# Kernel tuning notes

Hardware: AMD Instinct MI355X
Metric: run time of the kernel (lower is better)

Reference implementation:

```python
import jax, jax.numpy as jnp
import numpy as np

N = 4096
NUM_FEATURES = 1870
HIDDEN = 256
EMBED = 16
ALPHA = 0.2
NEG_BIG = -9e15
EPS = 1e-12


def setup_inputs() -> dict:
    key = jax.random.key(0)
    ks = jax.random.split(key, 9)
    x = jax.random.normal(ks[0], (N, NUM_FEATURES), dtype=jnp.float32)
    # sparse-ish binary adjacency mask (avg degree ~ 41) with self loops
    adj = (jax.random.uniform(ks[1], (N, N)) < 0.01).astype(jnp.float32)
    adj = jnp.maximum(adj, jnp.eye(N, dtype=jnp.float32))
    M = jax.random.uniform(ks[2], (N, N), dtype=jnp.float32)
    s1 = 1.0 / np.sqrt(NUM_FEATURES)
    s2 = 1.0 / np.sqrt(HIDDEN)
    W1 = jax.random.normal(ks[3], (NUM_FEATURES, HIDDEN), dtype=jnp.float32) * s1
    a_self1 = jax.random.normal(ks[4], (HIDDEN, 1), dtype=jnp.float32) * s2
    a_neighs1 = jax.random.normal(ks[5], (HIDDEN, 1), dtype=jnp.float32) * s2
    W2 = jax.random.normal(ks[6], (HIDDEN, EMBED), dtype=jnp.float32) * s2
    a_self2 = jax.random.normal(ks[7], (EMBED, 1), dtype=jnp.float32) / np.sqrt(EMBED)
    a_neighs2 = jax.random.normal(ks[8], (EMBED, 1), dtype=jnp.float32) / np.sqrt(EMBED)
    return {"x": x, "adj": adj, "M": M, "W1": W1, "a_self1": a_self1,
            "a_neighs1": a_neighs1, "W2": W2, "a_self2": a_self2, "a_neighs2": a_neighs2}


def gat_layer(x, adj, M, W, a_self, a_neighs, alpha):
    h = x @ W                                  # [N, out]
    f_self = h @ a_self                        # [N, 1]
    f_neigh = h @ a_neighs                     # [N, 1]
    e = jax.nn.leaky_relu((f_self + f_neigh.T) * M, negative_slope=alpha)  # [N, N]
    e = jnp.where(adj > 0, e, NEG_BIG)
    att = jax.nn.softmax(e, axis=1)            # row-stochastic over neighbors
    return jax.nn.elu(att @ h)                 # [N, out]


def reference(x, adj, M, W1, a_self1, a_neighs1, W2, a_self2, a_neighs2):
    h = gat_layer(x, adj, M, W1, a_self1, a_neighs1, ALPHA)
    h = gat_layer(h, adj, M, W2, a_self2, a_neighs2, ALPHA)
    # F.normalize(h, p=2, dim=1): divide by max(norm, eps)
    norm = jnp.maximum(jnp.linalg.norm(h, axis=1, keepdims=True), EPS)
    z = h / norm                               # [N, EMBED]
    A_pred = jax.nn.sigmoid(z @ z.T)           # [N, N]
    return (A_pred, z)
```

## Files before the change

kernel.cpp:

```cpp
#include <hip/hip_runtime.h>
#include <math.h>

#define NN 4096
#define NFEAT 1870
#define KB 1920
#define KSPLIT 4
#define KCHUNK 480
#define NSTEP 15
#define HID 256
#define EMB 16
#define MAXDEG 128

typedef __attribute__((ext_vector_type(8))) _Float16 f16x8;
typedef __attribute__((ext_vector_type(4))) float f32x4;

__device__ __forceinline__ ushort f2h(float f) {
    _Float16 h = (_Float16)f;
    return __builtin_bit_cast(ushort, h);
}

struct af32 { float2 v[4]; };

__device__ __forceinline__ af32 load_a_raw(const float* __restrict__ rp, int k0) {
    af32 r;
    if (k0 + 8 <= NFEAT) {
#pragma unroll
        for (int j = 0; j < 4; ++j) r.v[j] = *(const float2*)&rp[k0 + j * 2];
    } else {
#pragma unroll
        for (int j = 0; j < 4; ++j) {
            float a = (k0 + j * 2     < NFEAT) ? rp[k0 + j * 2]     : 0.f;
            float b = (k0 + j * 2 + 1 < NFEAT) ? rp[k0 + j * 2 + 1] : 0.f;
            r.v[j] = make_float2(a, b);
        }
    }
    return r;
}
__device__ __forceinline__ f16x8 cvt_a(af32 r) {
    f16x8 o;
#pragma unroll
    for (int j = 0; j < 4; ++j) {
        o[j * 2]     = (_Float16)r.v[j].x;
        o[j * 2 + 1] = (_Float16)r.v[j].y;
    }
    return o;
}

__global__ __launch_bounds__(256) void prep_kernel(
    const float* __restrict__ W1, ushort* __restrict__ Wh,
    const float* __restrict__ adj, const float* __restrict__ Mmat,
    int* __restrict__ nnz, int* __restrict__ gidx, float* __restrict__ Mg)
{
    const int b = blockIdx.x;
    const int tid = threadIdx.x;
    if (b < NN) {
        const int row = b;
        const int lane = tid & 63, wv = tid >> 6;
        const float* arow = adj + (size_t)row * NN + tid * 16;
        float4 v[4];
#pragma unroll
        for (int i = 0; i < 4; ++i) v[i] = *(const float4*)&arow[i * 4];
        unsigned mask = 0;
#pragma unroll
        for (int i = 0; i < 4; ++i) {
            if (v[i].x > 0.f) mask |= 1u << (i * 4 + 0);
            if (v[i].y > 0.f) mask |= 1u << (i * 4 + 1);
            if (v[i].z > 0.f) mask |= 1u << (i * 4 + 2);
            if (v[i].w > 0.f) mask |= 1u << (i * 4 + 3);
        }
        const int cnt = __popc(mask);
        int incl = cnt;
#pragma unroll
        for (int off = 1; off < 64; off <<= 1) {
            int y = __shfl_up(incl, off, 64);
            if (lane >= off) incl += y;
        }
        __shared__ int wsums[4];
        if (lane == 63) wsums[wv] = incl;
        __syncthreads();
        int base = incl - cnt;
#pragma unroll
        for (int i = 0; i < 4; ++i)
            if (i < wv) base += wsums[i];
        if (tid == 0) {
            int total = wsums[0] + wsums[1] + wsums[2] + wsums[3];
            nnz[row] = min(total, MAXDEG);
        }
        unsigned mm = mask;
        int off = base;
        while (mm) {
            int bit = __ffs(mm) - 1;
            mm &= mm - 1;
            if (off < MAXDEG) {
                int j = tid * 16 + bit;
                gidx[(size_t)row * MAXDEG + off] = j;
                Mg[(size_t)row * MAXDEG + off] = Mmat[(size_t)row * NN + j];
            }
            ++off;
        }
    } else {
        __shared__ float t[64][65];
        const int bb = b - NN;
        const int k0 = (bb % 30) * 64, n0 = (bb / 30) * 64;
        const int kk = tid >> 2, c4 = (tid & 3) * 16;
#pragma unroll
        for (int j = 0; j < 4; ++j) {
            int k = k0 + kk;
            float4 v = make_float4(0.f, 0.f, 0.f, 0.f);
            if (k < NFEAT) v = *(const float4*)&W1[(size_t)k * HID + n0 + c4 + j * 4];
            t[kk][c4 + j * 4 + 0] = v.x; t[kk][c4 + j * 4 + 1] = v.y;
            t[kk][c4 + j * 4 + 2] = v.z; t[kk][c4 + j * 4 + 3] = v.w;
        }
        __syncthreads();
        const int on = tid >> 2, ok4 = (tid & 3) * 16;
#pragma unroll
        for (int j = 0; j < 4; ++j) {
            ushort hh[4];
#pragma unroll
            for (int i = 0; i < 4; ++i)
                hh[i] = f2h(t[ok4 + j * 4 + i][on]);
            size_t o = (size_t)(n0 + on) * KB + k0 + ok4 + j * 4;
            *(ushort4*)&Wh[o] = *(ushort4*)hh;
        }
    }
}

__global__ __launch_bounds__(256, 4) void gemm_xw1(
    const float* __restrict__ Xg,
    const ushort* __restrict__ Bg,
    float* __restrict__ Cpart)
{
    const int tid = threadIdx.x;
    const int lane = tid & 63;
    const int cgrp = tid >> 6;
    const int mgrp = blockIdx.x >> 2;
    const int z    = blockIdx.x & 3;
    const int row0 = mgrp * 16;
    const int col0 = cgrp * 64;
    const int kbeg = z * KCHUNK;
    const int fr = lane & 15, fs = lane >> 4;

    const float* Arow = Xg + (size_t)(row0 + fr) * NFEAT;
    const ushort* Bbase = Bg + (size_t)(col0 + fr) * KB + kbeg + fs * 8;

    af32 araw = load_a_raw(Arow, kbeg + fs * 8);
    f16x8 bc[4];
#pragma unroll
    for (int n = 0; n < 4; ++n)
        bc[n] = *(const f16x8*)&Bbase[(size_t)n * 16 * KB];

    f32x4 acc[4] = {};
#pragma unroll
    for (int sk = 0; sk < NSTEP; ++sk) {
        f16x8 ac = cvt_a(araw);
        af32 anxt;
        f16x8 bn[4];
        if (sk + 1 < NSTEP) {
            anxt = load_a_raw(Arow, kbeg + (sk + 1) * 32 + fs * 8);
#pragma unroll
            for (int n = 0; n < 4; ++n)
                bn[n] = *(const f16x8*)&Bbase[(size_t)n * 16 * KB + (sk + 1) * 32];
        }
#pragma unroll
        for (int n = 0; n < 4; ++n)
            acc[n] = __builtin_amdgcn_mfma_f32_16x16x32_f16(ac, bc[n], acc[n], 0, 0, 0);
        if (sk + 1 < NSTEP) {
            araw = anxt;
#pragma unroll
            for (int n = 0; n < 4; ++n) bc[n] = bn[n];
        }
    }
    float* Cp = Cpart + (size_t)z * NN * HID;
#pragma unroll
    for (int n = 0; n < 4; ++n)
#pragma unroll
        for (int r = 0; r < 4; ++r) {
            int row = row0 + fs * 4 + r;
            int col = col0 + n * 16 + fr;
            Cp[(size_t)row * HID + col] = acc[n][r];
        }
}

__global__ __launch_bounds__(256) void reduce_h1f_kernel(
    const float* __restrict__ part, float* __restrict__ h1,
    const float* __restrict__ a_s, const float* __restrict__ a_n,
    float* __restrict__ fs, float* __restrict__ fn)
{
    const int tid = threadIdx.x, wv = tid >> 6, lane = tid & 63;
    const int row = blockIdx.x * 4 + wv;
    const int d0 = lane * 4;
    const size_t o = (size_t)row * HID + d0;
    float4 s = *(const float4*)&part[o];
#pragma unroll
    for (int ch = 1; ch < KSPLIT; ++ch) {
        float4 p = *(const float4*)&part[(size_t)ch * NN * HID + o];
        s.x += p.x; s.y += p.y; s.z += p.z; s.w += p.w;
    }
    *(float4*)&h1[o] = s;
    float4 as4 = *(const float4*)&a_s[d0];
    float4 an4 = *(const float4*)&a_n[d0];
    float ps = s.x * as4.x + s.y * as4.y + s.z * as4.z + s.w * as4.w;
    float pn = s.x * an4.x + s.y * an4.y + s.z * an4.z + s.w * an4.w;
#pragma unroll
    for (int off = 32; off > 0; off >>= 1) {
        ps += __shfl_down(ps, off, 64);
        pn += __shfl_down(pn, off, 64);
    }
    if (lane == 0) { fs[row] = ps; fn[row] = pn; }
}

__global__ __launch_bounds__(256) void spmm1_kernel(
    const int* __restrict__ nnz, const int* __restrict__ gidx,
    const float* __restrict__ Mg,
    const float* __restrict__ fs, const float* __restrict__ fn,
    const float* __restrict__ h1, float* __restrict__ g1)
{
    __shared__ float p_s[MAXDEG];
    __shared__ int j_s[MAXDEG];
    __shared__ float wred[4], wsum[4];
    const int row = blockIdx.x;
    const int tid = threadIdx.x;
    const int lane = tid & 63, wv = tid >> 6;
    const int cnt = nnz[row];
    const float fsi = fs[row];

    float lmax = -3.0e38f;
    for (int s = tid; s < cnt; s += 256) {
        int j = gidx[(size_t)row * MAXDEG + s];
        j_s[s] = j;
        float e = (fsi + fn[j]) * Mg[(size_t)row * MAXDEG + s];
        e = (e > 0.f) ? e : 0.2f * e;
        p_s[s] = e;
        lmax = fmaxf(lmax, e);
    }
#pragma unroll
    for (int off = 32; off > 0; off >>= 1)
        lmax = fmaxf(lmax, __shfl_down(lmax, off, 64));
    if (lane == 0) wred[wv] = lmax;
    __syncthreads();
    const float m = fmaxf(fmaxf(wred[0], wred[1]), fmaxf(wred[2], wred[3]));

    float lsum = 0.f;
    for (int s = tid; s < cnt; s += 256) {
        float p = __expf(p_s[s] - m);
        p_s[s] = p;
        lsum += p;
    }
#pragma unroll
    for (int off = 32; off > 0; off >>= 1)
        lsum += __shfl_down(lsum, off, 64);
    if (lane == 0) wsum[wv] = lsum;
    __syncthreads();
    const float inv = 1.f / (wsum[0] + wsum[1] + wsum[2] + wsum[3]);

    float acc = 0.f;
#pragma unroll 4
    for (int s = 0; s < cnt; ++s)
        acc += p_s[s] * h1[(size_t)j_s[s] * HID + tid];
    float v = acc * inv;
    v = (v > 0.f) ? v : (__expf(v) - 1.f);
    g1[(size_t)row * HID + tid] = v;
}

__global__ __launch_bounds__(256) void gemm_h2_kernel(
    const float* __restrict__ g1, const float* __restrict__ W2,
    const float* __restrict__ a_s2, const float* __restrict__ a_n2,
    float* __restrict__ h2, float* __restrict__ fs2, float* __restrict__ fn2)
{
    __shared__ float Ws[256][16];
    __shared__ float Gs[16][257];
    const int tid = threadIdx.x;
    const int row0 = blockIdx.x * 16;
#pragma unroll
    for (int i = 0; i < 16; ++i) {
        int idx = tid + i * 256;
        Ws[idx >> 4][idx & 15] = W2[idx];
    }
#pragma unroll
    for (int i = 0; i < 16; ++i) {
        int idx = tid + i * 256;
        Gs[idx >> 8][idx & 255] = g1[(size_t)(row0 + (idx >> 8)) * HID + (idx & 255)];
    }
    __syncthreads();
    const int r = tid >> 4, c = tid & 15;
    float acc = 0.f;
#pragma unroll 8
    for (int k = 0; k < 256; ++k)
        acc += Gs[r][k] * Ws[k][c];
    h2[(size_t)(row0 + r) * EMB + c] = acc;

    float ps = acc * a_s2[c];
    float pn = acc * a_n2[c];
#pragma unroll
    for (int off = 1; off < 16; off <<= 1) {
        ps += __shfl_xor(ps, off, 64);
        pn += __shfl_xor(pn, off, 64);
    }
    if (c == 0) { fs2[row0 + r] = ps; fn2[row0 + r] = pn; }
}

__global__ __launch_bounds__(256) void spmm2_kernel(
    const int* __restrict__ nnz, const int* __restrict__ gidx,
    const float* __restrict__ Mg,
    const float* __restrict__ fs, const float* __restrict__ fn,
    const float* __restrict__ h2, float* __restrict__ z)
{
    __shared__ float p_s[4][MAXDEG];
    __shared__ int j_s[4][MAXDEG];
    const int tid = threadIdx.x;
    const int wv = tid >> 6, lane = tid & 63;
    const int row = blockIdx.x * 4 + wv;
    const int cnt = nnz[row];
    const float fsi = fs[row];

    float lmax = -3.0e38f;
    for (int s = lane; s < cnt; s += 64) {
        int j = gidx[(size_t)row * MAXDEG + s];
        j_s[wv][s] = j;
        float e = (fsi + fn[j]) * Mg[(size_t)row * MAXDEG + s];
        e = (e > 0.f) ? e : 0.2f * e;
        p_s[wv][s] = e;
        lmax = fmaxf(lmax, e);
    }
#pragma unroll
    for (int off = 1; off < 64; off <<= 1)
        lmax = fmaxf(lmax, __shfl_xor(lmax, off, 64));

    float lsum = 0.f;
    for (int s = lane; s < cnt; s += 64) {
        float p = __expf(p_s[wv][s] - lmax);
        p_s[wv][s] = p;
        lsum += p;
    }
#pragma unroll
    for (int off = 1; off < 64; off <<= 1)
        lsum += __shfl_xor(lsum, off, 64);
    const float inv = 1.f / lsum;

    const int s0 = lane >> 4, d = lane & 15;
    float acc = 0.f;
    for (int s = s0; s < cnt; s += 4)
        acc += p_s[wv][s] * h2[(size_t)j_s[wv][s] * EMB + d];
    acc += __shfl_xor(acc, 16, 64);
    acc += __shfl_xor(acc, 32, 64);

    float v = acc * inv;
    v = (v > 0.f) ? v : (__expf(v) - 1.f);
    float ss = v * v;
#pragma unroll
    for (int off = 1; off < 16; off <<= 1)
        ss += __shfl_xor(ss, off, 64);
    float zn = v / fmaxf(sqrtf(ss), 1e-12f);
    if (lane < 16) z[(size_t)row * EMB + lane] = zn;
}

__global__ __launch_bounds__(256) void apred_kernel(
    const float* __restrict__ z, float* __restrict__ out)
{
    __shared__ float zr[64][20];
    __shared__ float zc[64][20];
    const int tid = threadIdx.x;
    const int r0 = blockIdx.y * 64, c0 = blockIdx.x * 64;
#pragma unroll
    for (int i = 0; i < 4; ++i) {
        int idx = tid + i * 256;
        int rr = idx >> 4, d = idx & 15;
        zr[rr][d] = z[(size_t)(r0 + rr) * EMB + d];
        zc[rr][d] = z[(size_t)(c0 + rr) * EMB + d];
    }
    __syncthreads();
    const int tx = tid & 15, ty = tid >> 4;
    float rb[4][16], cb[4][16];
#pragma unroll
    for (int i = 0; i < 4; ++i)
#pragma unroll
        for (int d = 0; d < 16; ++d) {
            rb[i][d] = zr[ty * 4 + i][d];
            cb[i][d] = zc[tx * 4 + i][d];
        }
#pragma unroll
    for (int i = 0; i < 4; ++i) {
        float4 o;
        float v[4];
#pragma unroll
        for (int j = 0; j < 4; ++j) {
            float s = 0.f;
#pragma unroll
            for (int d = 0; d < 16; ++d) s += rb[i][d] * cb[j][d];
            v[j] = 1.f / (1.f + __expf(-s));
        }
        o.x = v[0]; o.y = v[1]; o.z = v[2]; o.w = v[3];
        *reinterpret_cast<float4*>(
            &out[(size_t)(r0 + ty * 4 + i) * NN + c0 + tx * 4]) = o;
    }
}

extern "C" void kernel_launch(void* const* d_in, const int* in_sizes, int n_in,
                              void* d_out, int out_size, void* d_ws, size_t ws_size,
                              hipStream_t stream)
{
    const float* x    = (const float*)d_in[0];
    const float* adj  = (const float*)d_in[1];
    const float* Mm   = (const float*)d_in[2];
    const float* W1   = (const float*)d_in[3];
    const float* a_s1 = (const float*)d_in[4];
    const float* a_n1 = (const float*)d_in[5];
    const float* W2   = (const float*)d_in[6];
    const float* a_s2 = (const float*)d_in[7];
    const float* a_n2 = (const float*)d_in[8];

    float* out = (float*)d_out;
    float* z   = out + (size_t)NN * NN;
    float* part = out;

    char* w = (char*)d_ws;
    float* h1    = (float*)w;  w += (size_t)NN * HID * 4;
    float* g1    = (float*)w;  w += (size_t)NN * HID * 4;
    ushort* W1Th = (ushort*)w; w += (size_t)HID * KB * 2;
    float* h2    = (float*)w;  w += (size_t)NN * EMB * 4;
    int*   nnzp  = (int*)w;    w += NN * 4;
    int*   gidx  = (int*)w;    w += (size_t)NN * MAXDEG * 4;
    float* Mg    = (float*)w;  w += (size_t)NN * MAXDEG * 4;
    float* fs1   = (float*)w;  w += NN * 4;
    float* fn1   = (float*)w;  w += NN * 4;
    float* fs2   = (float*)w;  w += NN * 4;
    float* fn2   = (float*)w;  w += NN * 4;

    prep_kernel<<<NN + 120, 256, 0, stream>>>(W1, W1Th, adj, Mm, nnzp, gidx, Mg);

    gemm_xw1<<<(NN / 16) * KSPLIT, 256, 0, stream>>>(x, W1Th, part);
    reduce_h1f_kernel<<<NN / 4, 256, 0, stream>>>(part, h1, a_s1, a_n1, fs1, fn1);
    spmm1_kernel<<<NN, 256, 0, stream>>>(nnzp, gidx, Mg, fs1, fn1, h1, g1);

    gemm_h2_kernel<<<256, 256, 0, stream>>>(g1, W2, a_s2, a_n2, h2, fs2, fn2);
    spmm2_kernel<<<NN / 4, 256, 0, stream>>>(nnzp, gidx, Mg, fs2, fn2, h2, z);

    apred_kernel<<<dim3(64, 64), 256, 0, stream>>>(z, out);
}
```

Measured before the change: 109.9 us.

## Pre-convert x to fp16 and use LDS-tiled 128x128 split-K MFMA GEMM

```diff
diff --git a/kernel.cpp b/kernel.cpp
--- a/kernel.cpp
+++ b/kernel.cpp
@@ -3,10 +3,10 @@
 
 #define NN 4096
 #define NFEAT 1870
-#define KB 1920
-#define KSPLIT 4
-#define KCHUNK 480
-#define NSTEP 15
+#define KB2 2048
+#define KSPLIT 8
+#define KCHUNK 256
+#define BK 32
 #define HID 256
 #define EMB 16
 #define MAXDEG 128
@@ -19,34 +19,14 @@
     return __builtin_bit_cast(ushort, h);
 }
 
-struct af32 { float2 v[4]; };
-
-__device__ __forceinline__ af32 load_a_raw(const float* __restrict__ rp, int k0) {
-    af32 r;
-    if (k0 + 8 <= NFEAT) {
-#pragma unroll
-        for (int j = 0; j < 4; ++j) r.v[j] = *(const float2*)&rp[k0 + j * 2];
-    } else {
-#pragma unroll
-        for (int j = 0; j < 4; ++j) {
-            float a = (k0 + j * 2     < NFEAT) ? rp[k0 + j * 2]     : 0.f;
-            float b = (k0 + j * 2 + 1 < NFEAT) ? rp[k0 + j * 2 + 1] : 0.f;
-            r.v[j] = make_float2(a, b);
-        }
-    }
-    return r;
-}
-__device__ __forceinline__ f16x8 cvt_a(af32 r) {
-    f16x8 o;
-#pragma unroll
-    for (int j = 0; j < 4; ++j) {
-        o[j * 2]     = (_Float16)r.v[j].x;
-        o[j * 2 + 1] = (_Float16)r.v[j].y;
-    }
-    return o;
+__device__ __forceinline__ void gload_lds16(const void* g, void* l) {
+    __builtin_amdgcn_global_load_lds(
+        (const __attribute__((address_space(1))) unsigned int*)g,
+        (__attribute__((address_space(3))) unsigned int*)l, 16, 0, 0);
 }
 
 __global__ __launch_bounds__(256) void prep_kernel(
+    const float* __restrict__ x, ushort* __restrict__ xf,
     const float* __restrict__ W1, ushort* __restrict__ Wh,
     const float* __restrict__ adj, const float* __restrict__ Mmat,
     int* __restrict__ nnz, int* __restrict__ gidx, float* __restrict__ Mg)
@@ -98,10 +78,29 @@
             }
             ++off;
         }
+    } else if (b < 2 * NN) {
+        const int row = b - NN;
+        const int c0 = tid * 8;
+        float v[8];
+        if (c0 + 8 <= NFEAT) {
+#pragma unroll
+            for (int j = 0; j < 4; ++j) {
+                float2 t = *(const float2*)&x[(size_t)row * NFEAT + c0 + j * 2];
+                v[j * 2] = t.x; v[j * 2 + 1] = t.y;
+            }
+        } else {
+#pragma unroll
+            for (int j = 0; j < 8; ++j)
+                v[j] = (c0 + j < NFEAT) ? x[(size_t)row * NFEAT + c0 + j] : 0.f;
+        }
+        ushort u[8];
+#pragma unroll
+        for (int j = 0; j < 8; ++j) u[j] = f2h(v[j]);
+        *(int4*)&xf[(size_t)row * KB2 + c0] = *(int4*)u;
     } else {
         __shared__ float t[64][65];
-        const int bb = b - NN;
-        const int k0 = (bb % 30) * 64, n0 = (bb / 30) * 64;
+        const int bb = b - 2 * NN;
+        const int k0 = (bb & 31) * 64, n0 = (bb >> 5) * 64;
         const int kk = tid >> 2, c4 = (tid & 3) * 16;
 #pragma unroll
         for (int j = 0; j < 4; ++j) {
@@ -119,66 +118,71 @@
 #pragma unroll
             for (int i = 0; i < 4; ++i)
                 hh[i] = f2h(t[ok4 + j * 4 + i][on]);
-            size_t o = (size_t)(n0 + on) * KB + k0 + ok4 + j * 4;
+            size_t o = (size_t)(n0 + on) * KB2 + k0 + ok4 + j * 4;
             *(ushort4*)&Wh[o] = *(ushort4*)hh;
         }
     }
 }
 
-__global__ __launch_bounds__(256, 4) void gemm_xw1(
-    const float* __restrict__ Xg,
+__global__ __launch_bounds__(256, 2) void gemm_xw1(
+    const ushort* __restrict__ Ag,
     const ushort* __restrict__ Bg,
     float* __restrict__ Cpart)
 {
+    __shared__ ushort Ah[128 * BK];
+    __shared__ ushort Bh[128 * BK];
     const int tid = threadIdx.x;
     const int lane = tid & 63;
-    const int cgrp = tid >> 6;
-    const int mgrp = blockIdx.x >> 2;
-    const int z    = blockIdx.x & 3;
-    const int row0 = mgrp * 16;
-    const int col0 = cgrp * 64;
-    const int kbeg = z * KCHUNK;
+    const int w = tid >> 6;
+    const int wr = w >> 1, wc = w & 1;
+    const int row0 = blockIdx.x * 128;
+    const int col0 = blockIdx.y * 128;
+    const int kbeg = blockIdx.z * KCHUNK;
     const int fr = lane & 15, fs = lane >> 4;
 
-    const float* Arow = Xg + (size_t)(row0 + fr) * NFEAT;
-    const ushort* Bbase = Bg + (size_t)(col0 + fr) * KB + kbeg + fs * 8;
-
-    af32 araw = load_a_raw(Arow, kbeg + fs * 8);
-    f16x8 bc[4];
-#pragma unroll
-    for (int n = 0; n < 4; ++n)
-        bc[n] = *(const f16x8*)&Bbase[(size_t)n * 16 * KB];
-
-    f32x4 acc[4] = {};
-#pragma unroll
-    for (int sk = 0; sk < NSTEP; ++sk) {
-        f16x8 ac = cvt_a(araw);
-        af32 anxt;
-        f16x8 bn[4];
-        if (sk + 1 < NSTEP) {
-            anxt = load_a_raw(Arow, kbeg + (sk + 1) * 32 + fs * 8);
+    f32x4 acc[4][4] = {};
+
+    for (int ks = 0; ks < KCHUNK / BK; ++ks) {
+        const int k0 = kbeg + ks * BK;
+        __syncthreads();
+#pragma unroll
+        for (int i = 0; i < 2; ++i) {
+            int idx = i * 256 + tid;
+            int r = idx >> 2, t = idx & 3;
+            int kslot = (t ^ (r & 3)) * 8;
+            gload_lds16(&Ag[(size_t)(row0 + r) * KB2 + k0 + kslot], &Ah[idx * 8]);
+            gload_lds16(&Bg[(size_t)(col0 + r) * KB2 + k0 + kslot], &Bh[idx * 8]);
+        }
+        __syncthreads();
+        f16x8 af[4], bf[4];
+#pragma unroll
+        for (int m = 0; m < 4; ++m) {
+            int r = wr * 64 + m * 16 + fr;
+            af[m] = *(const f16x8*)&Ah[r * BK + ((fs ^ (r & 3)) * 8)];
+        }
+#pragma unroll
+        for (int n = 0; n < 4; ++n) {
+            int r = wc * 64 + n * 16 + fr;
+            bf[n] = *(const f16x8*)&Bh[r * BK + ((fs ^ (r & 3)) * 8)];
+        }
+#pragma unroll
+        for (int m = 0; m < 4; ++m)
 #pragma unroll
             for (int n = 0; n < 4; ++n)
-                bn[n] = *(const f16x8*)&Bbase[(size_t)n * 16 * KB + (sk + 1) * 32];
-        }
+                acc[m][n] = __builtin_amdgcn_mfma_f32_16x16x32_f16(
+                    af[m], bf[n], acc[m][n], 0, 0, 0);
+    }
+    float* Cp = Cpart + (size_t)blockIdx.z * NN * HID;
+#pragma unroll
+    for (int m = 0; m < 4; ++m)
 #pragma unroll
         for (int n = 0; n < 4; ++n)
-            acc[n] = __builtin_amdgcn_mfma_f32_16x16x32_f16(ac, bc[n], acc[n], 0, 0, 0);
-        if (sk + 1 < NSTEP) {
-            araw = anxt;
-#pragma unroll
-            for (int n = 0; n < 4; ++n) bc[n] = bn[n];
-        }
-    }
-    float* Cp = Cpart + (size_t)z * NN * HID;
-#pragma unroll
-    for (int n = 0; n < 4; ++n)
-#pragma unroll
-        for (int r = 0; r < 4; ++r) {
-            int row = row0 + fs * 4 + r;
-            int col = col0 + n * 16 + fr;
-            Cp[(size_t)row * HID + col] = acc[n][r];
-        }
+#pragma unroll
+            for (int r = 0; r < 4; ++r) {
+                int row = row0 + wr * 64 + m * 16 + fs * 4 + r;
+                int col = col0 + wc * 64 + n * 16 + fr;
+                Cp[(size_t)row * HID + col] = acc[m][n][r];
+            }
 }
 
 __global__ __launch_bounds__(256) void reduce_h1f_kernel(
@@ -416,7 +420,8 @@
     char* w = (char*)d_ws;
     float* h1    = (float*)w;  w += (size_t)NN * HID * 4;
     float* g1    = (float*)w;  w += (size_t)NN * HID * 4;
-    ushort* W1Th = (ushort*)w; w += (size_t)HID * KB * 2;
+    ushort* xf16 = (ushort*)w; w += (size_t)NN * KB2 * 2;
+    ushort* W1Th = (ushort*)w; w += (size_t)HID * KB2 * 2;
     float* h2    = (float*)w;  w += (size_t)NN * EMB * 4;
     int*   nnzp  = (int*)w;    w += NN * 4;
     int*   gidx  = (int*)w;    w += (size_t)NN * MAXDEG * 4;
@@ -426,9 +431,10 @@
     float* fs2   = (float*)w;  w += NN * 4;
     float* fn2   = (float*)w;  w += NN * 4;
 
-    prep_kernel<<<NN + 120, 256, 0, stream>>>(W1, W1Th, adj, Mm, nnzp, gidx, Mg);
-
-    gemm_xw1<<<(NN / 16) * KSPLIT, 256, 0, stream>>>(x, W1Th, part);
+    prep_kernel<<<2 * NN + 128, 256, 0, stream>>>(
+        x, xf16, W1, W1Th, adj, Mm, nnzp, gidx, Mg);
+
+    gemm_xw1<<<dim3(32, 2, KSPLIT), 256, 0, stream>>>(xf16, W1Th, part);
     reduce_h1f_kernel<<<NN / 4, 256, 0, stream>>>(part, h1, a_s1, a_n1, fs1, fn1);
     spmm1_kernel<<<NN, 256, 0, stream>>>(nnzp, gidx, Mg, fs1, fn1, h1, g1);
 
```

Measured after the change: 95.09 us. 13.5% less time.
